# Performance work log

Hardware: AMD Instinct MI355X
Metric: run time of the kernel (lower is better)

Reference implementation:

```python
import jax, jax.numpy as jnp
import numpy as np
from jax import lax

L, H = 16384, 1024
EPS = 1e-5


def _ln(x, w, b):
    m = jnp.mean(x, axis=-1, keepdims=True)
    v = jnp.var(x, axis=-1, keepdims=True)
    return (x - m) * lax.rsqrt(v + EPS) * w + b


def setup_inputs() -> dict:
    key = jax.random.key(0)
    ks = jax.random.split(key, 12)
    s = 0.02
    return {
        "x": jax.random.normal(ks[0], (L, H), dtype=jnp.float32),
        "ln1_w": jnp.ones((H,), jnp.float32),
        "ln1_b": jnp.zeros((H,), jnp.float32),
        "W_in": jax.random.normal(ks[1], (H, H), jnp.float32) * s,
        "b_in": jnp.zeros((H,), jnp.float32),
        "W_gate": jax.random.normal(ks[2], (H, H), jnp.float32) * s,
        "b_gate": jnp.zeros((H,), jnp.float32),
        "W_out": jax.random.normal(ks[3], (H, H), jnp.float32) * s,
        "b_out": jnp.zeros((H,), jnp.float32),
        "state_decay": jnp.zeros((H,), jnp.float32),
        "ln2_w": jnp.ones((H,), jnp.float32),
        "ln2_b": jnp.zeros((H,), jnp.float32),
        "W_ff1": jax.random.normal(ks[4], (H, 2 * H), jnp.float32) * s,
        "b_ff1": jnp.zeros((2 * H,), jnp.float32),
        "W_ff2": jax.random.normal(ks[5], (2 * H, H), jnp.float32) * s,
        "b_ff2": jnp.zeros((H,), jnp.float32),
    }


def reference(x, ln1_w, ln1_b, W_in, b_in, W_gate, b_gate, W_out, b_out,
              state_decay, ln2_w, ln2_b, W_ff1, b_ff1, W_ff2, b_ff2):
    hidden = _ln(x, ln1_w, ln1_b)                       # [L,H]
    u = hidden @ W_in + b_in                            # [L,H]
    gate = jax.nn.sigmoid(hidden @ W_gate + b_gate)     # [L,H]
    decay = jax.nn.sigmoid(state_decay)                 # [H]

    def step(s, u_t):
        s = decay * s + u_t
        return s, s

    z = jnp.zeros((x.shape[1],), x.dtype)
    _, states_f = lax.scan(step, z, u)                  # forward recurrence
    _, states_b = lax.scan(step, z, u, reverse=True)    # backward recurrence
    state_out = 0.5 * (states_f + states_b) * gate

    x = x + state_out @ W_out + b_out
    h = _ln(x, ln2_w, ln2_b)
    x = x + jax.nn.silu(h @ W_ff1 + b_ff1) @ W_ff2 + b_ff2
    return x
```

## Files before the change

### kernel.cpp

```cpp
#include <hip/hip_runtime.h>
#include <hip/hip_bf16.h>
#include <hip/hip_fp16.h>

#define L_SEQ 16384
#define HDIM  1024
#define CH    32
#define NC    (L_SEQ / CH)

typedef _Float16 f16;
typedef _Float16 f16x8 __attribute__((ext_vector_type(8)));
typedef _Float16 f16x4 __attribute__((ext_vector_type(4)));
typedef float    f32x4 __attribute__((ext_vector_type(4)));

#define AS1(p) (const __attribute__((address_space(1))) void*)(p)
#define AS3(p) (__attribute__((address_space(3))) void*)(p)

__global__ __launch_bounds__(256) void wcvt_t(const float* __restrict__ in,
                                              f16* __restrict__ out, int K, int N) {
  __shared__ float tile[32][33];
  int n0 = blockIdx.x * 32, k0 = blockIdx.y * 32;
  int tx = threadIdx.x, ty = threadIdx.y;
#pragma unroll
  for (int i = 0; i < 4; i++) {
    int k = k0 + ty + i * 8;
    tile[ty + i * 8][tx] = in[(size_t)k * N + n0 + tx];
  }
  __syncthreads();
#pragma unroll
  for (int i = 0; i < 4; i++) {
    int n = n0 + ty + i * 8;
    out[(size_t)n * K + k0 + tx] = (f16)tile[tx][ty + i * 8];
  }
}

__global__ __launch_bounds__(256) void ln_k(const float* __restrict__ x,
                                            const float* __restrict__ w,
                                            const float* __restrict__ b,
                                            f16* __restrict__ out,
                                            f16* __restrict__ xcopy) {
  int row = blockIdx.x;
  int t = threadIdx.x;
  const float4* xr = (const float4*)(x + (size_t)row * HDIM);
  float4 v = xr[t];
  float s  = v.x + v.y + v.z + v.w;
  float s2 = v.x * v.x + v.y * v.y + v.z * v.z + v.w * v.w;
#pragma unroll
  for (int off = 32; off > 0; off >>= 1) {
    s  += __shfl_down(s, off);
    s2 += __shfl_down(s2, off);
  }
  __shared__ float red[8];
  int wid = t >> 6, lane = t & 63;
  if (lane == 0) { red[wid] = s; red[4 + wid] = s2; }
  __syncthreads();
  if (t == 0) {
    red[0] = red[0] + red[1] + red[2] + red[3];
    red[4] = red[4] + red[5] + red[6] + red[7];
  }
  __syncthreads();
  float mean = red[0] * (1.0f / HDIM);
  float var  = red[4] * (1.0f / HDIM) - mean * mean;
  float rstd = rsqrtf(var + 1e-5f);
  float4 ww = ((const float4*)w)[t];
  float4 bb = ((const float4*)b)[t];
  f16x4 o;
  o[0] = (f16)((v.x - mean) * rstd * ww.x + bb.x);
  o[1] = (f16)((v.y - mean) * rstd * ww.y + bb.y);
  o[2] = (f16)((v.z - mean) * rstd * ww.z + bb.z);
  o[3] = (f16)((v.w - mean) * rstd * ww.w + bb.w);
  ((f16x4*)(out + (size_t)row * HDIM))[t] = o;
  if (xcopy) {
    f16x4 c;
    c[0] = (f16)v.x; c[1] = (f16)v.y; c[2] = (f16)v.z; c[3] = (f16)v.w;
    ((f16x4*)(xcopy + (size_t)row * HDIM))[t] = c;
  }
}

__global__ __launch_bounds__(256) void ln_k16(const f16* __restrict__ x,
                                              const float* __restrict__ w,
                                              const float* __restrict__ b,
                                              f16* __restrict__ out) {
  int row = blockIdx.x;
  int t = threadIdx.x;
  f16x4 xv = ((const f16x4*)(x + (size_t)row * HDIM))[t];
  float4 v = {(float)xv[0], (float)xv[1], (float)xv[2], (float)xv[3]};
  float s  = v.x + v.y + v.z + v.w;
  float s2 = v.x * v.x + v.y * v.y + v.z * v.z + v.w * v.w;
#pragma unroll
  for (int off = 32; off > 0; off >>= 1) {
    s  += __shfl_down(s, off);
    s2 += __shfl_down(s2, off);
  }
  __shared__ float red[8];
  int wid = t >> 6, lane = t & 63;
  if (lane == 0) { red[wid] = s; red[4 + wid] = s2; }
  __syncthreads();
  if (t == 0) {
    red[0] = red[0] + red[1] + red[2] + red[3];
    red[4] = red[4] + red[5] + red[6] + red[7];
  }
  __syncthreads();
  float mean = red[0] * (1.0f / HDIM);
  float var  = red[4] * (1.0f / HDIM) - mean * mean;
  float rstd = rsqrtf(var + 1e-5f);
  float4 ww = ((const float4*)w)[t];
  float4 bb = ((const float4*)b)[t];
  f16x4 o;
  o[0] = (f16)((v.x - mean) * rstd * ww.x + bb.x);
  o[1] = (f16)((v.y - mean) * rstd * ww.y + bb.y);
  o[2] = (f16)((v.z - mean) * rstd * ww.z + bb.z);
  o[3] = (f16)((v.w - mean) * rstd * ww.w + bb.w);
  ((f16x4*)(out + (size_t)row * HDIM))[t] = o;
}

template <int MODE, int RESID, int OUTF16>
__global__ __launch_bounds__(256, 3) void gemm_bt(const f16* __restrict__ A,
                                                  const f16* __restrict__ BT,
                                                  const float* __restrict__ bias,
                                                  const float* __restrict__ bias2,
                                                  const f16* __restrict__ resid,
                                                  void* __restrict__ Cout,
                                                  void* __restrict__ Cout2,
                                                  int M, int N, int K) {
  __shared__ __align__(16) f16 As[128 * 32];
  __shared__ __align__(16) f16 Bs[128 * 32];
  const int tid  = threadIdx.x;
  const int lane = tid & 63, wid = tid >> 6;
  const int wm = wid >> 1, wn = wid & 1;
  const int quad = lane >> 4, l16 = lane & 15;

  const int nbx = N >> 7, nby = M >> 7;
  const int b = blockIdx.x;
  const int xcd = b & 7;
  const int i = b >> 3;
  const int strips = nby >> 3;
  const int rs = i / nbx, cb = i - rs * nbx;
  const long m0 = (long)(xcd * strips + rs) << 7;
  const long n0 = (long)cb << 7;

  f32x4 zero = {0.f, 0.f, 0.f, 0.f};
  f32x4 acc[4][4];
#pragma unroll
  for (int i2 = 0; i2 < 4; i2++)
#pragma unroll
    for (int j = 0; j < 4; j++) acc[i2][j] = zero;

  for (int k0 = 0; k0 < K; k0 += 32) {
#pragma unroll
    for (int it = 0; it < 2; ++it) {
      int wboff = it * 4096 + wid * 1024;
      int eoff  = (wboff + lane * 16) >> 1;
      int r = eoff >> 5, c = eoff & 31;
      const f16* gA = A  + (m0 + r) * K + k0 + c;
      const f16* gB = BT + (n0 + r) * K + k0 + c;
      __builtin_amdgcn_global_load_lds(AS1(gA), AS3((char*)As + wboff), 16, 0, 0);
      __builtin_amdgcn_global_load_lds(AS1(gB), AS3((char*)Bs + wboff), 16, 0, 0);
    }
    __syncthreads();
    f16x8 af[4], bfr[4];
#pragma unroll
    for (int mi = 0; mi < 4; ++mi)
      af[mi] = *(const f16x8*)(As + (wm * 64 + mi * 16 + l16) * 32 + quad * 8);
#pragma unroll
    for (int ni = 0; ni < 4; ++ni)
      bfr[ni] = *(const f16x8*)(Bs + (wn * 64 + ni * 16 + l16) * 32 + quad * 8);
#pragma unroll
    for (int mi = 0; mi < 4; ++mi)
#pragma unroll
      for (int ni = 0; ni < 4; ++ni)
        acc[mi][ni] = __builtin_amdgcn_mfma_f32_16x16x32_f16(af[mi], bfr[ni], acc[mi][ni], 0, 0, 0);
    __syncthreads();
  }
#pragma unroll
  for (int mi = 0; mi < 4; ++mi) {
#pragma unroll
    for (int ni = 0; ni < 4; ++ni) {
      const long col = n0 + wn * 64 + ni * 16 + l16;
      float bc;
      if (MODE == 3) bc = (col < HDIM) ? bias[col] : bias2[col - HDIM];
      else           bc = bias[col];
#pragma unroll
      for (int r = 0; r < 4; ++r) {
        const long row = m0 + wm * 64 + mi * 16 + quad * 4 + r;
        float v = acc[mi][ni][r] + bc;
        if (MODE == 2) v = v / (1.f + __expf(-v));
        if (MODE == 3) {
          if (col < HDIM) {
            ((f16*)Cout)[row * HDIM + col] = (f16)v;
          } else {
            float g = 1.f / (1.f + __expf(-v));
            ((f16*)Cout2)[row * HDIM + (col - HDIM)] = (f16)g;
          }
        } else {
          if (RESID) v += (float)resid[row * N + col];
          if (OUTF16) ((f16*)Cout)[row * N + col] = (f16)v;
          else        ((float*)Cout)[row * N + col] = v;
        }
      }
    }
  }
}

__global__ __launch_bounds__(256) void scan_p1(const f16* __restrict__ u,
                                               const float* __restrict__ sdecay,
                                               float* __restrict__ carry_f,
                                               float* __restrict__ carry_b) {
  int tid = blockIdx.x * 256 + threadIdx.x;
  int h = tid & (HDIM - 1);
  int c = tid >> 10;
  float d = 1.f / (1.f + expf(-sdecay[h]));
  const f16* up = u + (size_t)c * CH * HDIM + h;
  float sf = 0.f, sb = 0.f, p = 1.f;
#pragma unroll
  for (int i = 0; i < CH; i++) {
    float uu = (float)up[i * HDIM];
    sf = d * sf + uu;
    sb += p * uu;
    p *= d;
  }
  carry_f[(size_t)c * HDIM + h] = sf;
  carry_b[(size_t)c * HDIM + h] = sb;
}

__global__ __launch_bounds__(256) void scan_p2(const float* __restrict__ sdecay,
                                               const float* __restrict__ carry_f,
                                               const float* __restrict__ carry_b,
                                               float* __restrict__ cin_f,
                                               float* __restrict__ cin_b) {
  int tid = blockIdx.x * 256 + threadIdx.x;
  int h = tid & (HDIM - 1);
  int dir = tid >> 10;
  float d = 1.f / (1.f + expf(-sdecay[h]));
  float dT = powf(d, (float)CH);
  float S = 0.f;
  if (dir == 0) {
#pragma unroll 4
    for (int c = 0; c < NC; c++) {
      cin_f[(size_t)c * HDIM + h] = S;
      S = dT * S + carry_f[(size_t)c * HDIM + h];
    }
  } else {
#pragma unroll 4
    for (int c = NC - 1; c >= 0; c--) {
      cin_b[(size_t)c * HDIM + h] = S;
      S = dT * S + carry_b[(size_t)c * HDIM + h];
    }
  }
}

__global__ __launch_bounds__(256) void scan_p3(const f16* __restrict__ u,
                                               const f16* __restrict__ gate,
                                               const float* __restrict__ sdecay,
                                               const float* __restrict__ cin_f,
                                               const float* __restrict__ cin_b,
                                               f16* __restrict__ state_out) {
  int tid = blockIdx.x * 256 + threadIdx.x;
  int h = tid & (HDIM - 1);
  int c = tid >> 10;
  float d = 1.f / (1.f + expf(-sdecay[h]));
  const f16* up = u    + (size_t)c * CH * HDIM + h;
  const f16* gp = gate + (size_t)c * CH * HDIM + h;
  f16* op = state_out  + (size_t)c * CH * HDIM + h;
  float ur[CH], sf[CH];
#pragma unroll
  for (int i = 0; i < CH; i++) ur[i] = (float)up[i * HDIM];
  float s = cin_f[(size_t)c * HDIM + h];
#pragma unroll
  for (int i = 0; i < CH; i++) { s = d * s + ur[i]; sf[i] = s; }
  s = cin_b[(size_t)c * HDIM + h];
#pragma unroll
  for (int i = CH - 1; i >= 0; i--) {
    s = d * s + ur[i];
    float g = (float)gp[i * HDIM];
    op[i * HDIM] = (f16)(0.5f * (sf[i] + s) * g);
  }
}

extern "C" void kernel_launch(void* const* d_in, const int* in_sizes, int n_in,
                              void* d_out, int out_size, void* d_ws, size_t ws_size,
                              hipStream_t stream) {
  const float* x      = (const float*)d_in[0];
  const float* ln1_w  = (const float*)d_in[1];
  const float* ln1_b  = (const float*)d_in[2];
  const float* W_in   = (const float*)d_in[3];
  const float* b_in   = (const float*)d_in[4];
  const float* W_gate = (const float*)d_in[5];
  const float* b_gate = (const float*)d_in[6];
  const float* W_out  = (const float*)d_in[7];
  const float* b_out  = (const float*)d_in[8];
  const float* sdecay = (const float*)d_in[9];
  const float* ln2_w  = (const float*)d_in[10];
  const float* ln2_b  = (const float*)d_in[11];
  const float* W_ff1  = (const float*)d_in[12];
  const float* b_ff1  = (const float*)d_in[13];
  const float* W_ff2  = (const float*)d_in[14];
  const float* b_ff2  = (const float*)d_in[15];
  float* out = (float*)d_out;

  char* ws = (char*)d_ws;
  const size_t MB32 = 33554432, MB64 = 67108864;
  f16* hidden = (f16*)(ws);
  f16* xh     = (f16*)(ws + MB32);
  f16* u      = (f16*)(ws + 2 * MB32);
  f16* gate   = (f16*)(ws + 3 * MB32);
  f16* x2h    = (f16*)(ws + 4 * MB32);
  f16* ff     = (f16*)(ws + 5 * MB32);
  char* wbase = ws + 5 * MB32 + MB64;
  f16* wt_ug  = (f16*)(wbase);
  f16* wt_out = (f16*)(wbase + 4194304);
  f16* wt_ff1 = (f16*)(wbase + 4194304 + 2097152);
  f16* wt_ff2 = (f16*)(wbase + 2 * 4194304 + 2097152);
  char* cbase = wbase + 3 * 4194304 + 2097152;
  float* carry_f = (float*)(cbase);
  float* carry_b = (float*)(cbase + 2097152);
  float* cin_f   = (float*)(cbase + 2 * 2097152);
  float* cin_b   = (float*)(cbase + 3 * 2097152);
  f16* state_out = hidden;
  f16* h2        = u;

  dim3 tb(32, 8);
  wcvt_t<<<dim3(32, 32), tb, 0, stream>>>(W_in,   wt_ug,                 1024, 1024);
  wcvt_t<<<dim3(32, 32), tb, 0, stream>>>(W_gate, wt_ug + 1024 * 1024,   1024, 1024);
  wcvt_t<<<dim3(32, 32), tb, 0, stream>>>(W_out,  wt_out,                1024, 1024);
  wcvt_t<<<dim3(64, 32), tb, 0, stream>>>(W_ff1,  wt_ff1,                1024, 2048);
  wcvt_t<<<dim3(32, 64), tb, 0, stream>>>(W_ff2,  wt_ff2,                2048, 1024);

  ln_k<<<L_SEQ, 256, 0, stream>>>(x, ln1_w, ln1_b, hidden, xh);

  gemm_bt<3, 0, 1><<<2048, 256, 0, stream>>>(hidden, wt_ug, b_in, b_gate, nullptr,
                                             u, gate, L_SEQ, 2048, 1024);

  scan_p1<<<2048, 256, 0, stream>>>(u, sdecay, carry_f, carry_b);
  scan_p2<<<8, 256, 0, stream>>>(sdecay, carry_f, carry_b, cin_f, cin_b);
  scan_p3<<<2048, 256, 0, stream>>>(u, gate, sdecay, cin_f, cin_b, state_out);

  gemm_bt<0, 1, 1><<<1024, 256, 0, stream>>>(state_out, wt_out, b_out, nullptr, xh,
                                             x2h, nullptr, L_SEQ, 1024, 1024);

  ln_k16<<<L_SEQ, 256, 0, stream>>>(x2h, ln2_w, ln2_b, h2);

  gemm_bt<2, 0, 1><<<2048, 256, 0, stream>>>(h2, wt_ff1, b_ff1, nullptr, nullptr,
                                             ff, nullptr, L_SEQ, 2048, 1024);

  gemm_bt<0, 1, 0><<<1024, 256, 0, stream>>>(ff, wt_ff2, b_ff2, nullptr, x2h,
                                             out, nullptr, L_SEQ, 1024, 2048);
}
```

Baseline: 600.2 us.

## Swizzle GEMM LDS tiles, raise occupancy hint, and widen LN2 kernel

The GEMM now loads each 16-byte chunk of the A and B tiles from a column position XOR-permuted by the row index, and reads fragments back with the same XOR. The aim is to cut LDS bank conflicts on the fragment reads. The launch-bounds occupancy hint rises from 3 to 4 blocks per CU, which may force register spilling. The second layer norm now uses 128 threads with 8-wide f16 loads and a single barrier, to reduce reduction and synchronisation overhead.

```diff
diff --git a/kernel.cpp b/kernel.cpp
--- a/kernel.cpp
+++ b/kernel.cpp
@@ -76,45 +76,44 @@
   }
 }
 
-__global__ __launch_bounds__(256) void ln_k16(const f16* __restrict__ x,
+__global__ __launch_bounds__(128) void ln_k16(const f16* __restrict__ x,
                                               const float* __restrict__ w,
                                               const float* __restrict__ b,
                                               f16* __restrict__ out) {
   int row = blockIdx.x;
   int t = threadIdx.x;
-  f16x4 xv = ((const f16x4*)(x + (size_t)row * HDIM))[t];
-  float4 v = {(float)xv[0], (float)xv[1], (float)xv[2], (float)xv[3]};
-  float s  = v.x + v.y + v.z + v.w;
-  float s2 = v.x * v.x + v.y * v.y + v.z * v.z + v.w * v.w;
+  f16x8 xv = ((const f16x8*)(x + (size_t)row * HDIM))[t];
+  float v[8];
+  float s = 0.f, s2 = 0.f;
+#pragma unroll
+  for (int i = 0; i < 8; i++) {
+    v[i] = (float)xv[i];
+    s += v[i]; s2 += v[i] * v[i];
+  }
 #pragma unroll
   for (int off = 32; off > 0; off >>= 1) {
     s  += __shfl_down(s, off);
     s2 += __shfl_down(s2, off);
   }
-  __shared__ float red[8];
+  __shared__ float red[4];
   int wid = t >> 6, lane = t & 63;
-  if (lane == 0) { red[wid] = s; red[4 + wid] = s2; }
+  if (lane == 0) { red[wid] = s; red[2 + wid] = s2; }
   __syncthreads();
-  if (t == 0) {
-    red[0] = red[0] + red[1] + red[2] + red[3];
-    red[4] = red[4] + red[5] + red[6] + red[7];
-  }
-  __syncthreads();
-  float mean = red[0] * (1.0f / HDIM);
-  float var  = red[4] * (1.0f / HDIM) - mean * mean;
+  float mean = (red[0] + red[1]) * (1.0f / HDIM);
+  float var  = (red[2] + red[3]) * (1.0f / HDIM) - mean * mean;
   float rstd = rsqrtf(var + 1e-5f);
-  float4 ww = ((const float4*)w)[t];
-  float4 bb = ((const float4*)b)[t];
-  f16x4 o;
-  o[0] = (f16)((v.x - mean) * rstd * ww.x + bb.x);
-  o[1] = (f16)((v.y - mean) * rstd * ww.y + bb.y);
-  o[2] = (f16)((v.z - mean) * rstd * ww.z + bb.z);
-  o[3] = (f16)((v.w - mean) * rstd * ww.w + bb.w);
-  ((f16x4*)(out + (size_t)row * HDIM))[t] = o;
+  float4 w1 = ((const float4*)w)[2 * t], w2 = ((const float4*)w)[2 * t + 1];
+  float4 b1 = ((const float4*)b)[2 * t], b2 = ((const float4*)b)[2 * t + 1];
+  float wv[8] = {w1.x, w1.y, w1.z, w1.w, w2.x, w2.y, w2.z, w2.w};
+  float bv[8] = {b1.x, b1.y, b1.z, b1.w, b2.x, b2.y, b2.z, b2.w};
+  f16x8 o;
+#pragma unroll
+  for (int i = 0; i < 8; i++) o[i] = (f16)((v[i] - mean) * rstd * wv[i] + bv[i]);
+  ((f16x8*)(out + (size_t)row * HDIM))[t] = o;
 }
 
 template <int MODE, int RESID, int OUTF16>
-__global__ __launch_bounds__(256, 3) void gemm_bt(const f16* __restrict__ A,
+__global__ __launch_bounds__(256, 4) void gemm_bt(const f16* __restrict__ A,
                                                   const f16* __restrict__ BT,
                                                   const float* __restrict__ bias,
                                                   const float* __restrict__ bias2,
@@ -150,20 +149,26 @@
     for (int it = 0; it < 2; ++it) {
       int wboff = it * 4096 + wid * 1024;
       int eoff  = (wboff + lane * 16) >> 1;
-      int r = eoff >> 5, c = eoff & 31;
-      const f16* gA = A  + (m0 + r) * K + k0 + c;
-      const f16* gB = BT + (n0 + r) * K + k0 + c;
+      int r = eoff >> 5;
+      int chunk = lane & 3;
+      int src_c = ((chunk ^ (r & 3)) << 3);
+      const f16* gA = A  + (m0 + r) * K + k0 + src_c;
+      const f16* gB = BT + (n0 + r) * K + k0 + src_c;
       __builtin_amdgcn_global_load_lds(AS1(gA), AS3((char*)As + wboff), 16, 0, 0);
       __builtin_amdgcn_global_load_lds(AS1(gB), AS3((char*)Bs + wboff), 16, 0, 0);
     }
     __syncthreads();
     f16x8 af[4], bfr[4];
 #pragma unroll
-    for (int mi = 0; mi < 4; ++mi)
-      af[mi] = *(const f16x8*)(As + (wm * 64 + mi * 16 + l16) * 32 + quad * 8);
-#pragma unroll
-    for (int ni = 0; ni < 4; ++ni)
-      bfr[ni] = *(const f16x8*)(Bs + (wn * 64 + ni * 16 + l16) * 32 + quad * 8);
+    for (int mi = 0; mi < 4; ++mi) {
+      int row = wm * 64 + mi * 16 + l16;
+      af[mi] = *(const f16x8*)(As + row * 32 + ((quad ^ (row & 3)) << 3));
+    }
+#pragma unroll
+    for (int ni = 0; ni < 4; ++ni) {
+      int row = wn * 64 + ni * 16 + l16;
+      bfr[ni] = *(const f16x8*)(Bs + row * 32 + ((quad ^ (row & 3)) << 3));
+    }
 #pragma unroll
     for (int mi = 0; mi < 4; ++mi)
 #pragma unroll
@@ -337,7 +342,7 @@
   gemm_bt<0, 1, 1><<<1024, 256, 0, stream>>>(state_out, wt_out, b_out, nullptr, xh,
                                              x2h, nullptr, L_SEQ, 1024, 1024);
 
-  ln_k16<<<L_SEQ, 256, 0, stream>>>(x2h, ln2_w, ln2_b, h2);
+  ln_k16<<<L_SEQ, 128, 0, stream>>>(x2h, ln2_w, ln2_b, h2);
 
   gemm_bt<2, 0, 1><<<2048, 256, 0, stream>>>(h2, wt_ff1, b_ff1, nullptr, nullptr,
                                              ff, nullptr, L_SEQ, 2048, 1024);
```

Result: no change. 599.0 us (-0.2%).
